# Optimization experiments

Measured on AMD Instinct MI355X. Metric: run time of the kernel, lower is better.

## Reference

```python
import jax, jax.numpy as jnp
import numpy as np

N = 100000
E = 3200000
F_IN = 128
H1, H2 = 32, 16
R = 8
G = 512  # number of graphs in batch


def setup_inputs() -> dict:
    key = jax.random.key(0)
    ks = jax.random.split(key, 12)
    x = jax.random.normal(ks[0], (N, F_IN), dtype=jnp.float32)
    edge_index = jax.random.randint(ks[1], (2, E), 0, N, dtype=jnp.int64)
    edge_attr = jax.random.randint(ks[2], (E,), 0, R, dtype=jnp.int64)
    batch = jnp.sort(jax.random.randint(ks[3], (N,), 0, G, dtype=jnp.int64))
    s1 = 1.0 / np.sqrt(F_IN)
    s2 = 1.0 / np.sqrt(H1)
    s3 = 1.0 / np.sqrt(H2)
    W1 = jax.random.uniform(ks[4], (R, F_IN, H1), jnp.float32, -s1, s1)
    root1 = jax.random.uniform(ks[5], (F_IN, H1), jnp.float32, -s1, s1)
    b1 = jnp.zeros((H1,), jnp.float32)
    W2 = jax.random.uniform(ks[6], (R, H1, H2), jnp.float32, -s2, s2)
    root2 = jax.random.uniform(ks[7], (H1, H2), jnp.float32, -s2, s2)
    b2 = jnp.zeros((H2,), jnp.float32)
    dense_w = jax.random.uniform(ks[8], (H2, 1), jnp.float32, -s3, s3)
    dense_b = jax.random.uniform(ks[9], (1,), jnp.float32, -s3, s3)
    return dict(x=x, edge_index=edge_index, edge_attr=edge_attr, batch=batch,
                W1=W1, root1=root1, b1=b1, W2=W2, root2=root2, b2=b2,
                dense_w=dense_w, dense_b=dense_b)


def rgcn_layer(x, W, root, b, src, dst, rel, num_rel):
    # Per-relation transform of all nodes: [N, R, out]
    xw = jnp.einsum('ni,rio->nro', x, W)
    msgs = xw[src, rel]                      # gather per edge: [E, out]
    seg = dst * num_rel + rel                # (node, relation) segment id
    nr = x.shape[0] * num_rel
    sums = jax.ops.segment_sum(msgs, seg, num_segments=nr)
    cnt = jax.ops.segment_sum(jnp.ones(src.shape, x.dtype), seg, num_segments=nr)
    mean = sums / jnp.maximum(cnt, 1.0)[:, None]
    agg = mean.reshape(x.shape[0], num_rel, -1).sum(axis=1)  # sum over relations
    return agg + x @ root + b


def reference(x, edge_index, edge_attr, batch, W1, root1, b1, W2, root2, b2, dense_w, dense_b):
    src, dst = edge_index[0], edge_index[1]
    rel = edge_attr
    h = jax.nn.relu(rgcn_layer(x, W1, root1, b1, src, dst, rel, R))
    # F.dropout is treated as identity (inference) for a deterministic reference
    h = jax.nn.relu(rgcn_layer(h, W2, root2, b2, src, dst, rel, R))
    pooled = jax.ops.segment_max(h, batch, num_segments=G)
    pooled = jnp.where(jnp.isfinite(pooled), pooled, 0.0)  # empty graphs -> 0
    return pooled @ dense_w + dense_b
```

## Files before the change

### kernel.cpp

```cpp
#include <hip/hip_runtime.h>
#include <hip/hip_bf16.h>

#define RNUM 8
#define HH1 32
#define HH2 16
#define FIN 128
#define BNODES 256
#define NBMAX 512
#define PCHUNK 8192
#define SORTCAP 11264

#define W1STR 136
#define W1ELTS (288 * W1STR)
#define W2STR 40
#define W2ELTS (144 * W2STR)

typedef short bf16x8 __attribute__((ext_vector_type(8)));
typedef float f32x4 __attribute__((ext_vector_type(4)));

__device__ inline bf16x8 cvt8r(float4 a, float4 b) {
  float tmp[8] = {a.x, a.y, a.z, a.w, b.x, b.y, b.z, b.w};
  bf16x8 r;
  #pragma unroll
  for (int j = 0; j < 8; ++j) {
    union { __hip_bfloat16 h; short s; } cv;
    cv.h = __float2bfloat16(tmp[j]);
    r[j] = cv.s;
  }
  return r;
}

__device__ inline bf16x8 cvt8relu(const float* __restrict__ p) {
  float tmp[8];
  *(float4*)tmp = *(const float4*)p;
  *(float4*)(tmp + 4) = *(const float4*)(p + 4);
  bf16x8 r;
  #pragma unroll
  for (int j = 0; j < 8; ++j) {
    union { __hip_bfloat16 h; short s; } cv;
    cv.h = __float2bfloat16(fmaxf(tmp[j], 0.f));
    r[j] = cv.s;
  }
  return r;
}

__device__ inline uint2 pack4bf(f32x4 v) {
  union { unsigned short u[4]; uint2 w; } pk;
  union { __hip_bfloat16 h; unsigned short s; } cv;
  cv.h = __float2bfloat16(v[0]); pk.u[0] = cv.s;
  cv.h = __float2bfloat16(v[1]); pk.u[1] = cv.s;
  cv.h = __float2bfloat16(v[2]); pk.u[2] = cv.s;
  cv.h = __float2bfloat16(v[3]); pk.u[3] = cv.s;
  return pk.w;
}

__global__ __launch_bounds__(256) void k_bhist(const int* __restrict__ ei,
    int* __restrict__ ghist, int E, int NB) {
  __shared__ int h[NBMAX];
  int t = threadIdx.x;
  for (int i = t; i < NBMAX; i += 256) h[i] = 0;
  __syncthreads();
  int base = blockIdx.x * 4096;
  #pragma unroll
  for (int j = 0; j < 16; ++j) {
    int e = base + j * 256 + t;
    if (e < E) atomicAdd(&h[ei[E + e] >> 8], 1);
  }
  __syncthreads();
  for (int i = t; i < NB; i += 256)
    if (h[i]) atomicAdd(&ghist[i], h[i]);
}

__global__ __launch_bounds__(NBMAX) void k_bscan(const int* __restrict__ ghist,
    int* __restrict__ bbase, int* __restrict__ gcursor, int NB, int E) {
  __shared__ int buf[NBMAX];
  int t = threadIdx.x;
  int v = (t < NB) ? ghist[t] : 0;
  buf[t] = v;
  __syncthreads();
  for (int d = 1; d < NBMAX; d <<= 1) {
    int w = (t >= d) ? buf[t - d] : 0;
    __syncthreads();
    buf[t] += w;
    __syncthreads();
  }
  if (t < NB) {
    int ex = buf[t] - v;
    bbase[t] = ex;
    gcursor[t] = ex;
  }
  if (t == 0) bbase[NB] = E;
}

__global__ __launch_bounds__(512) void k_part(const int* __restrict__ ei,
    const int* __restrict__ ea, int* __restrict__ gcursor,
    unsigned* __restrict__ ebuf, int E, int NB) {
  __shared__ unsigned reorder[PCHUNK];
  __shared__ unsigned short bkt[PCHUNK];
  __shared__ int hist[NBMAX], startl[NBMAX], cursor[NBMAX], gb[NBMAX], scanb[NBMAX];
  int t = threadIdx.x;
  int base = blockIdx.x * PCHUNK;
  int cn = min(PCHUNK, E - base);
  unsigned key[16];
  short bb[16];
  hist[t] = 0;
  __syncthreads();
  #pragma unroll
  for (int j = 0; j < 16; ++j) {
    int e = base + j * 512 + t;
    bb[j] = -1;
    if (e < E) {
      int src = ei[e], dst = ei[E + e], rel = ea[e];
      key[j] = ((unsigned)(dst & (BNODES - 1)) << 20) | ((unsigned)src << 3) | (unsigned)rel;
      int b = dst >> 8;
      bb[j] = (short)b;
      atomicAdd(&hist[b], 1);
    }
  }
  __syncthreads();
  int v = hist[t];
  scanb[t] = v;
  __syncthreads();
  for (int d = 1; d < NBMAX; d <<= 1) {
    int w = (t >= d) ? scanb[t - d] : 0;
    __syncthreads();
    scanb[t] += w;
    __syncthreads();
  }
  startl[t] = scanb[t] - v;
  cursor[t] = scanb[t] - v;
  __syncthreads();
  #pragma unroll
  for (int j = 0; j < 16; ++j) {
    if (bb[j] >= 0) {
      int pos = atomicAdd(&cursor[bb[j]], 1);
      reorder[pos] = key[j];
      bkt[pos] = (unsigned short)bb[j];
    }
  }
  __syncthreads();
  if (t < NB && hist[t] > 0) gb[t] = atomicAdd(&gcursor[t], hist[t]);
  __syncthreads();
  for (int p = t; p < cn; p += 512) {
    int b = bkt[p];
    ebuf[gb[b] + (p - startl[b])] = reorder[p];
  }
}

__global__ __launch_bounds__(512) void k_sort(const int* __restrict__ bbase,
    const unsigned* __restrict__ ebuf, unsigned* __restrict__ ebuf2,
    float* __restrict__ wbuf, int* __restrict__ rps, int* __restrict__ rpc,
    int NB) {
  __shared__ int hist[2048];
  __shared__ float invw[2048];
  __shared__ int dlc[256];
  __shared__ unsigned sorted[SORTCAP];
  int t = threadIdx.x;
  int b = blockIdx.x;
  int s = bbase[b], e = bbase[b + 1];
  int out_s = ((s + 7) & ~7) + (b << 11);
  for (int i = t; i < 2048; i += 512) hist[i] = 0;
  __syncthreads();
  for (int p = s + t; p < e; p += 512) {
    unsigned k = ebuf[p];
    atomicAdd(&hist[((k >> 20) << 3) | (k & 7u)], 1);
  }
  __syncthreads();
  for (int i = t; i < 2048; i += 512) {
    int c = hist[i];
    invw[i] = 1.0f / (float)(c > 1 ? c : 1);
  }
  __syncthreads();
  int pr[8];
  int cdl = 0, pc = 0;
  if (t < 256) {
    #pragma unroll
    for (int r = 0; r < 8; ++r) { pr[r] = cdl; cdl += hist[8 * t + r]; }
    pc = (cdl + 7) & ~7;
    dlc[t] = pc;
  }
  __syncthreads();
  for (int d = 1; d < 256; d <<= 1) {
    int w = (t < 256 && t >= d) ? dlc[t - d] : 0;
    __syncthreads();
    if (t < 256) dlc[t] += w;
    __syncthreads();
  }
  if (t < 256) {
    int ebase = dlc[t] - pc;
    #pragma unroll
    for (int r = 0; r < 8; ++r) hist[8 * t + r] = ebase + pr[r];
    rps[(b << 8) + t] = out_s + ebase;
    rpc[(b << 8) + t] = cdl;
  }
  __syncthreads();
  int ptot = dlc[255];
  if (ptot <= SORTCAP) {
    for (int p = t; p < ptot; p += 512) sorted[p] = 0xFFFFFFFFu;
    __syncthreads();
    for (int p = s + t; p < e; p += 512) {
      unsigned k = ebuf[p];
      int pos = atomicAdd(&hist[((k >> 20) << 3) | (k & 7u)], 1);
      sorted[pos] = k;
    }
    __syncthreads();
    for (int p = t; p < ptot; p += 512) {
      unsigned k = sorted[p];
      int o = out_s + p;
      if (k == 0xFFFFFFFFu) { ebuf2[o] = 0u; wbuf[o] = 0.f; }
      else { ebuf2[o] = k; wbuf[o] = invw[((k >> 20) << 3) | (k & 7u)]; }
    }
  } else {
    if (t < 256) {
      int ebase = dlc[t] - pc;
      for (int p = ebase + cdl; p < dlc[t]; ++p) {
        ebuf2[out_s + p] = 0u; wbuf[out_s + p] = 0.f;
      }
    }
    __syncthreads();
    for (int p = s + t; p < e; p += 512) {
      unsigned k = ebuf[p];
      int bin = ((k >> 20) << 3) | (k & 7u);
      int pos = atomicAdd(&hist[bin], 1);
      ebuf2[out_s + pos] = k;
      wbuf[out_s + pos] = invw[bin];
    }
  }
}

__global__ __launch_bounds__(256) void k_prepw(const float* __restrict__ W1,
    const float* __restrict__ root1, const float* __restrict__ W2,
    const float* __restrict__ root2, unsigned short* __restrict__ Wcat,
    unsigned short* __restrict__ W2cat) {
  int id = blockIdx.x * 256 + threadIdx.x;
  union { __hip_bfloat16 h; unsigned short u; } cv;
  if (id < W1ELTS) {
    int c = id / W1STR, kk = id - c * W1STR;
    float v = 0.f;
    if (kk < FIN)
      v = (c < 256) ? W1[((size_t)(c >> 5) * FIN + kk) * HH1 + (c & 31)]
                    : root1[(size_t)kk * HH1 + (c - 256)];
    cv.h = __float2bfloat16(v);
    Wcat[id] = cv.u;
  } else if (id < W1ELTS + W2ELTS) {
    int id2 = id - W1ELTS;
    int c = id2 / W2STR, kk = id2 - c * W2STR;
    float v = 0.f;
    if (kk < HH1)
      v = (c < 128) ? W2[((size_t)(c >> 4) * HH1 + kk) * HH2 + (c & 15)]
                    : root2[(size_t)kk * HH2 + (c - 128)];
    cv.h = __float2bfloat16(v);
    W2cat[id2] = cv.u;
  }
}

__global__ __launch_bounds__(384) void k_gemm1m(const float* __restrict__ x,
    const unsigned short* __restrict__ Wcat, const float* __restrict__ b1,
    __hip_bfloat16* __restrict__ xw, float* __restrict__ agg, int N, int nchunk) {
  int lane = threadIdx.x & 63;
  int wv = threadIdx.x >> 6;
  int g = lane >> 4, lc = lane & 15;
  int cj0 = wv * 3;
  bf16x8 Wf[3][4];
  #pragma unroll
  for (int j = 0; j < 3; ++j)
    #pragma unroll
    for (int ks = 0; ks < 4; ++ks)
      Wf[j][ks] = *(const bf16x8*)(Wcat + (size_t)((cj0 + j) * 16 + lc) * W1STR + ks * 32 + g * 8);

  for (int ch = blockIdx.x; ch < nchunk; ch += gridDim.x) {
    long base = (long)ch * 32;
    long r0 = base + lc;       if (r0 > N - 1) r0 = N - 1;
    long r1 = base + 16 + lc;  if (r1 > N - 1) r1 = N - 1;
    const float4* p0 = (const float4*)(x + r0 * FIN + g * 8);
    const float4* p1 = (const float4*)(x + r1 * FIN + g * 8);
    float4 raw[16];
    #pragma unroll
    for (int ks = 0; ks < 4; ++ks) {
      raw[2 * ks]     = p0[ks * 8];
      raw[2 * ks + 1] = p0[ks * 8 + 1];
    }
    #pragma unroll
    for (int ks = 0; ks < 4; ++ks) {
      raw[8 + 2 * ks]     = p1[ks * 8];
      raw[8 + 2 * ks + 1] = p1[ks * 8 + 1];
    }
    bf16x8 xf0[4], xf1[4];
    #pragma unroll
    for (int ks = 0; ks < 4; ++ks) {
      xf0[ks] = cvt8r(raw[2 * ks], raw[2 * ks + 1]);
      xf1[ks] = cvt8r(raw[8 + 2 * ks], raw[8 + 2 * ks + 1]);
    }
    f32x4 acc0[3], acc1[3];
    #pragma unroll
    for (int j = 0; j < 3; ++j) {
      acc0[j] = (f32x4){0.f, 0.f, 0.f, 0.f};
      acc1[j] = (f32x4){0.f, 0.f, 0.f, 0.f};
    }
    #pragma unroll
    for (int j = 0; j < 3; ++j)
      #pragma unroll
      for (int ks = 0; ks < 4; ++ks) {
        acc0[j] = __builtin_amdgcn_mfma_f32_16x16x32_bf16(Wf[j][ks], xf0[ks], acc0[j], 0, 0, 0);
        acc1[j] = __builtin_amdgcn_mfma_f32_16x16x32_bf16(Wf[j][ks], xf1[ks], acc1[j], 0, 0, 0);
      }
    long row0 = base + lc;
    if (row0 < N) {
      #pragma unroll
      for (int j = 0; j < 3; ++j) {
        int c0 = (cj0 + j) * 16 + 4 * g;
        if (c0 < 256) {
          *(uint2*)((unsigned short*)xw + row0 * 256 + c0) = pack4bf(acc0[j]);
        } else {
          float4 bb = *(const float4*)(b1 + (c0 - 256));
          float4 o = make_float4(acc0[j][0] + bb.x, acc0[j][1] + bb.y,
                                 acc0[j][2] + bb.z, acc0[j][3] + bb.w);
          *(float4*)(agg + row0 * HH1 + (c0 - 256)) = o;
        }
      }
    }
    long row1 = base + 16 + lc;
    if (row1 < N) {
      #pragma unroll
      for (int j = 0; j < 3; ++j) {
        int c0 = (cj0 + j) * 16 + 4 * g;
        if (c0 < 256) {
          *(uint2*)((unsigned short*)xw + row1 * 256 + c0) = pack4bf(acc1[j]);
        } else {
          float4 bb = *(const float4*)(b1 + (c0 - 256));
          float4 o = make_float4(acc1[j][0] + bb.x, acc1[j][1] + bb.y,
                                 acc1[j][2] + bb.z, acc1[j][3] + bb.w);
          *(float4*)(agg + row1 * HH1 + (c0 - 256)) = o;
        }
      }
    }
  }
}

__global__ __launch_bounds__(256) void k_agg1(const int* __restrict__ rps,
    const int* __restrict__ rpc, const unsigned* __restrict__ eb,
    const float* __restrict__ wb, const __hip_bfloat16* __restrict__ xw,
    float* __restrict__ agg, int N) {
  int d = blockIdx.x * 4 + (threadIdx.x >> 6);
  if (d >= N) return;
  int lane = threadIdx.x & 63;
  int h = lane & 31, half = lane >> 5;
  int s = rps[d];
  int cnt = rpc[d];
  float acc = 0.f;
  for (int j = half * 8; j < cnt; j += 16) {
    const unsigned* kp = eb + s + j;
    uint4 ka = *(const uint4*)kp;
    uint4 kb = *(const uint4*)(kp + 4);
    float4 wa = *(const float4*)(wb + s + j);
    float4 wc = *(const float4*)(wb + s + j + 4);
    unsigned ks[8] = {ka.x, ka.y, ka.z, ka.w, kb.x, kb.y, kb.z, kb.w};
    float ws[8] = {wa.x, wa.y, wa.z, wa.w, wc.x, wc.y, wc.z, wc.w};
    #pragma unroll
    for (int u = 0; u < 8; ++u) {
      unsigned idx = ks[u] & 0xFFFFFu;
      float v = __bfloat162float(xw[((size_t)idx << 5) + h]);
      acc = fmaf(ws[u], v, acc);
    }
  }
  acc += __shfl_xor(acc, 32);
  if (half == 0) agg[((size_t)d << 5) + h] += acc;
}

__global__ __launch_bounds__(384) void k_gemm2m(const float* __restrict__ agg1,
    const unsigned short* __restrict__ W2cat, const float* __restrict__ b2,
    __hip_bfloat16* __restrict__ xw, float* __restrict__ agg, int N) {
  __shared__ short WL[W2ELTS];
  __shared__ short XT[192 * 132];
  __shared__ float AG[192 * 20];
  int t = threadIdx.x;
  for (int i = t; i < W2ELTS / 8; i += 384)
    ((uint4*)WL)[i] = ((const uint4*)W2cat)[i];
  __syncthreads();
  int lane = t & 63;
  int wv = t >> 6;
  int g = lane >> 4, lc = lane & 15;
  long nb = (long)blockIdx.x * 192 + wv * 32;
  f32x4 acc[2][9];
  #pragma unroll
  for (int m = 0; m < 2; ++m)
    #pragma unroll
    for (int j = 0; j < 9; ++j)
      acc[m][j] = (f32x4){0.f, 0.f, 0.f, 0.f};
  long rowA0 = nb + lc;       if (rowA0 > N - 1) rowA0 = N - 1;
  long rowA1 = nb + 16 + lc;  if (rowA1 > N - 1) rowA1 = N - 1;
  bf16x8 a0 = cvt8relu(agg1 + rowA0 * HH1 + g * 8);
  bf16x8 a1 = cvt8relu(agg1 + rowA1 * HH1 + g * 8);
  #pragma unroll
  for (int j = 0; j < 9; ++j) {
    bf16x8 bf = *(const bf16x8*)(WL + (16 * j + lc) * W2STR + g * 8);
    acc[0][j] = __builtin_amdgcn_mfma_f32_16x16x32_bf16(bf, a0, acc[0][j], 0, 0, 0);
    acc[1][j] = __builtin_amdgcn_mfma_f32_16x16x32_bf16(bf, a1, acc[1][j], 0, 0, 0);
  }
  #pragma unroll
  for (int m = 0; m < 2; ++m) {
    int lrow = wv * 32 + 16 * m + lc;
    #pragma unroll
    for (int j = 0; j < 8; ++j)
      *(uint2*)(XT + lrow * 132 + 16 * j + 4 * g) = pack4bf(acc[m][j]);
    float4 bb = *(const float4*)(b2 + 4 * g);
    *(float4*)(AG + lrow * 20 + 4 * g) =
        make_float4(acc[m][8][0] + bb.x, acc[m][8][1] + bb.y,
                    acc[m][8][2] + bb.z, acc[m][8][3] + bb.w);
  }
  __syncthreads();
  long base = (long)blockIdx.x * 192;
  for (int i = t; i < 6144; i += 384) {
    int row = i >> 5, u = i & 31;
    long grow = base + row;
    if (grow < N)
      *(uint2*)((unsigned short*)xw + grow * 128 + u * 4) = *(const uint2*)(XT + row * 132 + u * 4);
  }
  for (int i = t; i < 768; i += 384) {
    int row = i >> 2, q = i & 3;
    long grow = base + row;
    if (grow < N)
      *(float4*)(agg + grow * HH2 + q * 4) = *(const float4*)(AG + row * 20 + q * 4);
  }
}

__global__ __launch_bounds__(256) void k_agg2f(const int* __restrict__ rps,
    const int* __restrict__ rpc, const unsigned* __restrict__ eb,
    const float* __restrict__ wb, const __hip_bfloat16* __restrict__ xw,
    const float* __restrict__ agg2r, const int* __restrict__ batch,
    unsigned* __restrict__ pooled, int N) {
  int d = blockIdx.x * 4 + (threadIdx.x >> 6);
  if (d >= N) return;
  int lane = threadIdx.x & 63;
  int h = lane & 15, q = lane >> 4;
  int s = rps[d];
  int cnt = rpc[d];
  float acc = 0.f;
  for (int j = q * 8; j < cnt; j += 32) {
    const unsigned* kp = eb + s + j;
    uint4 ka = *(const uint4*)kp;
    uint4 kb = *(const uint4*)(kp + 4);
    float4 wa = *(const float4*)(wb + s + j);
    float4 wc = *(const float4*)(wb + s + j + 4);
    unsigned ks[8] = {ka.x, ka.y, ka.z, ka.w, kb.x, kb.y, kb.z, kb.w};
    float ws[8] = {wa.x, wa.y, wa.z, wa.w, wc.x, wc.y, wc.z, wc.w};
    #pragma unroll
    for (int u = 0; u < 8; ++u) {
      unsigned idx = ks[u] & 0xFFFFFu;
      float v = __bfloat162float(xw[((size_t)idx << 4) + h]);
      acc = fmaf(ws[u], v, acc);
    }
  }
  acc += __shfl_xor(acc, 32);
  acc += __shfl_xor(acc, 16);
  if (q == 0) {
    float v = fmaxf(acc + agg2r[((size_t)d << 4) + h], 0.f);
    atomicMax(&pooled[batch[d] * HH2 + h], __float_as_uint(v));
  }
}

__global__ __launch_bounds__(256) void k_dense(const float* __restrict__ pooled,
    const float* __restrict__ dw, const float* __restrict__ db,
    float* __restrict__ out, int Gn) {
  int g = blockIdx.x * 256 + threadIdx.x;
  if (g < Gn) {
    float s = db[0];
    #pragma unroll
    for (int h = 0; h < HH2; ++h) s += pooled[(size_t)g * HH2 + h] * dw[h];
    out[g] = s;
  }
}

extern "C" void kernel_launch(void* const* d_in, const int* in_sizes, int n_in,
                              void* d_out, int out_size, void* d_ws, size_t ws_size,
                              hipStream_t stream) {
  const float* x     = (const float*)d_in[0];
  const int*   ei    = (const int*)d_in[1];
  const int*   ea    = (const int*)d_in[2];
  const int*   batch = (const int*)d_in[3];
  const float* W1    = (const float*)d_in[4];
  const float* root1 = (const float*)d_in[5];
  const float* b1    = (const float*)d_in[6];
  const float* W2    = (const float*)d_in[7];
  const float* root2 = (const float*)d_in[8];
  const float* b2    = (const float*)d_in[9];
  const float* dw    = (const float*)d_in[10];
  const float* db    = (const float*)d_in[11];
  float* out = (float*)d_out;

  const int N  = in_sizes[0] / FIN;
  const int E  = in_sizes[2];
  const int Gn = out_size;
  const int NB = (N + BNODES - 1) / BNODES;

  char* ws = (char*)d_ws;
  size_t off = 0;
  auto walloc = [&](size_t bytes) -> void* {
    void* p = (void*)(ws + off);
    off += (bytes + 255) & ~(size_t)255;
    return p;
  };
  const size_t EP = (size_t)E + (size_t)NBMAX * 2048 + 64;
  int*            ghist   = (int*)            walloc((size_t)NBMAX * 4);
  int*            bbase   = (int*)            walloc(((size_t)NBMAX + 1) * 4);
  int*            gcursor = (int*)            walloc((size_t)NBMAX * 4);
  unsigned*       ebuf    = (unsigned*)       walloc((size_t)E * 4);
  unsigned*       ebuf2   = (unsigned*)       walloc(EP * 4);
  float*          wbuf    = (float*)          walloc(EP * 4);
  int*            rps     = (int*)            walloc((size_t)NBMAX * 256 * 4);
  int*            rpc     = (int*)            walloc((size_t)NBMAX * 256 * 4);
  unsigned short* Wcat    = (unsigned short*) walloc((size_t)W1ELTS * 2);
  unsigned short* W2cat   = (unsigned short*) walloc((size_t)W2ELTS * 2);
  __hip_bfloat16* xw1     = (__hip_bfloat16*) walloc((size_t)N * RNUM * HH1 * 2);
  float*          agg1    = (float*)          walloc((size_t)N * HH1 * 4);
  __hip_bfloat16* xw2     = (__hip_bfloat16*) walloc((size_t)N * RNUM * HH2 * 2);
  float*          agg2r   = (float*)          walloc((size_t)N * HH2 * 4);
  unsigned*       pooled  = (unsigned*)       walloc((size_t)Gn * HH2 * 4);

  hipMemsetAsync(ghist, 0, (size_t)NBMAX * 4, stream);
  hipMemsetAsync(pooled, 0, (size_t)Gn * HH2 * 4, stream);

  k_prepw<<<(W1ELTS + W2ELTS + 255) / 256, 256, 0, stream>>>(W1, root1, W2, root2, Wcat, W2cat);
  k_bhist<<<(E + 4095) / 4096, 256, 0, stream>>>(ei, ghist, E, NB);
  k_bscan<<<1, NBMAX, 0, stream>>>(ghist, bbase, gcursor, NB, E);
  k_part<<<(E + PCHUNK - 1) / PCHUNK, 512, 0, stream>>>(ei, ea, gcursor, ebuf, E, NB);
  k_sort<<<NB, 512, 0, stream>>>(bbase, ebuf, ebuf2, wbuf, rps, rpc, NB);

  {
    int nchunk = (N + 31) / 32;
    k_gemm1m<<<nchunk, 384, 0, stream>>>(x, Wcat, b1, xw1, agg1, N, nchunk);
  }
  k_agg1<<<(N + 3) / 4, 256, 0, stream>>>(rps, rpc, ebuf2, wbuf, xw1, agg1, N);
  k_gemm2m<<<(N + 191) / 192, 384, 0, stream>>>(agg1, W2cat, b2, xw2, agg2r, N);
  k_agg2f<<<(N + 3) / 4, 256, 0, stream>>>(rps, rpc, ebuf2, wbuf, xw2,
                                           agg2r, batch, pooled, N);
  k_dense<<<(Gn + 255) / 256, 256, 0, stream>>>((const float*)pooled, dw, db, out, Gn);
}
```

Before: 276.3 us.

## Fuse bucket sort and layer-1 GEMM into one launch with block specialization

Merges the per-bucket edge sort kernel and the first-layer MFMA GEMM into a single launch. The first NB blocks do the sort and the remaining 512 blocks run a grid-strided GEMM, so the two independent stages can overlap and one launch is saved. The sort also drops its shared-memory staging path and always scatters directly to global memory, which frees LDS for occupancy but gives less coalesced writes. Fixing the GEMM grid at 512 blocks with 384 active threads out of 512 may leave some compute idle.

```diff
diff --git a/kernel.cpp b/kernel.cpp
--- a/kernel.cpp
+++ b/kernel.cpp
@@ -8,7 +8,7 @@
 #define BNODES 256
 #define NBMAX 512
 #define PCHUNK 8192
-#define SORTCAP 11264
+#define GEMMB 512
 
 #define W1STR 136
 #define W1ELTS (288 * W1STR)
@@ -147,74 +147,58 @@
   }
 }
 
-__global__ __launch_bounds__(512) void k_sort(const int* __restrict__ bbase,
-    const unsigned* __restrict__ ebuf, unsigned* __restrict__ ebuf2,
-    float* __restrict__ wbuf, int* __restrict__ rps, int* __restrict__ rpc,
-    int NB) {
+__global__ __launch_bounds__(512) void k_fuse2(
+    const int* __restrict__ bbase, const unsigned* __restrict__ ebuf,
+    unsigned* __restrict__ ebuf2, float* __restrict__ wbuf,
+    int* __restrict__ rps, int* __restrict__ rpc, int NB,
+    const float* __restrict__ x, const unsigned short* __restrict__ Wcat,
+    const float* __restrict__ b1, __hip_bfloat16* __restrict__ xw,
+    float* __restrict__ agg, int N, int nchunk) {
   __shared__ int hist[2048];
   __shared__ float invw[2048];
   __shared__ int dlc[256];
-  __shared__ unsigned sorted[SORTCAP];
   int t = threadIdx.x;
-  int b = blockIdx.x;
-  int s = bbase[b], e = bbase[b + 1];
-  int out_s = ((s + 7) & ~7) + (b << 11);
-  for (int i = t; i < 2048; i += 512) hist[i] = 0;
-  __syncthreads();
-  for (int p = s + t; p < e; p += 512) {
-    unsigned k = ebuf[p];
-    atomicAdd(&hist[((k >> 20) << 3) | (k & 7u)], 1);
-  }
-  __syncthreads();
-  for (int i = t; i < 2048; i += 512) {
-    int c = hist[i];
-    invw[i] = 1.0f / (float)(c > 1 ? c : 1);
-  }
-  __syncthreads();
-  int pr[8];
-  int cdl = 0, pc = 0;
-  if (t < 256) {
-    #pragma unroll
-    for (int r = 0; r < 8; ++r) { pr[r] = cdl; cdl += hist[8 * t + r]; }
-    pc = (cdl + 7) & ~7;
-    dlc[t] = pc;
-  }
-  __syncthreads();
-  for (int d = 1; d < 256; d <<= 1) {
-    int w = (t < 256 && t >= d) ? dlc[t - d] : 0;
-    __syncthreads();
-    if (t < 256) dlc[t] += w;
-    __syncthreads();
-  }
-  if (t < 256) {
-    int ebase = dlc[t] - pc;
-    #pragma unroll
-    for (int r = 0; r < 8; ++r) hist[8 * t + r] = ebase + pr[r];
-    rps[(b << 8) + t] = out_s + ebase;
-    rpc[(b << 8) + t] = cdl;
-  }
-  __syncthreads();
-  int ptot = dlc[255];
-  if (ptot <= SORTCAP) {
-    for (int p = t; p < ptot; p += 512) sorted[p] = 0xFFFFFFFFu;
+
+  if (blockIdx.x < NB) {
+    int b = blockIdx.x;
+    int s = bbase[b], e = bbase[b + 1];
+    int out_s = ((s + 7) & ~7) + (b << 11);
+    for (int i = t; i < 2048; i += 512) hist[i] = 0;
     __syncthreads();
     for (int p = s + t; p < e; p += 512) {
       unsigned k = ebuf[p];
-      int pos = atomicAdd(&hist[((k >> 20) << 3) | (k & 7u)], 1);
-      sorted[pos] = k;
-    }
-    __syncthreads();
-    for (int p = t; p < ptot; p += 512) {
-      unsigned k = sorted[p];
-      int o = out_s + p;
-      if (k == 0xFFFFFFFFu) { ebuf2[o] = 0u; wbuf[o] = 0.f; }
-      else { ebuf2[o] = k; wbuf[o] = invw[((k >> 20) << 3) | (k & 7u)]; }
-    }
-  } else {
+      atomicAdd(&hist[((k >> 20) << 3) | (k & 7u)], 1);
+    }
+    __syncthreads();
+    for (int i = t; i < 2048; i += 512) {
+      int c = hist[i];
+      invw[i] = 1.0f / (float)(c > 1 ? c : 1);
+    }
+    __syncthreads();
+    int pr[8];
+    int cdl = 0, pc = 0;
+    if (t < 256) {
+      #pragma unroll
+      for (int r = 0; r < 8; ++r) { pr[r] = cdl; cdl += hist[8 * t + r]; }
+      pc = (cdl + 7) & ~7;
+      dlc[t] = pc;
+    }
+    __syncthreads();
+    for (int d = 1; d < 256; d <<= 1) {
+      int w = (t < 256 && t >= d) ? dlc[t - d] : 0;
+      __syncthreads();
+      if (t < 256) dlc[t] += w;
+      __syncthreads();
+    }
     if (t < 256) {
       int ebase = dlc[t] - pc;
+      #pragma unroll
+      for (int r = 0; r < 8; ++r) hist[8 * t + r] = ebase + pr[r];
+      rps[(b << 8) + t] = out_s + ebase;
+      rpc[(b << 8) + t] = cdl;
       for (int p = ebase + cdl; p < dlc[t]; ++p) {
-        ebuf2[out_s + p] = 0u; wbuf[out_s + p] = 0.f;
+        ebuf2[out_s + p] = 0u;
+        wbuf[out_s + p] = 0.f;
       }
     }
     __syncthreads();
@@ -224,6 +208,88 @@
       int pos = atomicAdd(&hist[bin], 1);
       ebuf2[out_s + pos] = k;
       wbuf[out_s + pos] = invw[bin];
+    }
+    return;
+  }
+
+  if (t >= 384) return;
+  int lane = t & 63;
+  int wv = t >> 6;
+  int g = lane >> 4, lc = lane & 15;
+  int cj0 = wv * 3;
+  bf16x8 Wf[3][4];
+  #pragma unroll
+  for (int j = 0; j < 3; ++j)
+    #pragma unroll
+    for (int ks = 0; ks < 4; ++ks)
+      Wf[j][ks] = *(const bf16x8*)(Wcat + (size_t)((cj0 + j) * 16 + lc) * W1STR + ks * 32 + g * 8);
+
+  int gstride = gridDim.x - NB;
+  for (int ch = blockIdx.x - NB; ch < nchunk; ch += gstride) {
+    long base = (long)ch * 32;
+    long r0 = base + lc;       if (r0 > N - 1) r0 = N - 1;
+    long r1 = base + 16 + lc;  if (r1 > N - 1) r1 = N - 1;
+    const float4* p0 = (const float4*)(x + r0 * FIN + g * 8);
+    const float4* p1 = (const float4*)(x + r1 * FIN + g * 8);
+    float4 raw[16];
+    #pragma unroll
+    for (int ks = 0; ks < 4; ++ks) {
+      raw[2 * ks]     = p0[ks * 8];
+      raw[2 * ks + 1] = p0[ks * 8 + 1];
+    }
+    #pragma unroll
+    for (int ks = 0; ks < 4; ++ks) {
+      raw[8 + 2 * ks]     = p1[ks * 8];
+      raw[8 + 2 * ks + 1] = p1[ks * 8 + 1];
+    }
+    bf16x8 xf0[4], xf1[4];
+    #pragma unroll
+    for (int ks = 0; ks < 4; ++ks) {
+      xf0[ks] = cvt8r(raw[2 * ks], raw[2 * ks + 1]);
+      xf1[ks] = cvt8r(raw[8 + 2 * ks], raw[8 + 2 * ks + 1]);
+    }
+    f32x4 acc0[3], acc1[3];
+    #pragma unroll
+    for (int j = 0; j < 3; ++j) {
+      acc0[j] = (f32x4){0.f, 0.f, 0.f, 0.f};
+      acc1[j] = (f32x4){0.f, 0.f, 0.f, 0.f};
+    }
+    #pragma unroll
+    for (int j = 0; j < 3; ++j)
+      #pragma unroll
+      for (int ks = 0; ks < 4; ++ks) {
+        acc0[j] = __builtin_amdgcn_mfma_f32_16x16x32_bf16(Wf[j][ks], xf0[ks], acc0[j], 0, 0, 0);
+        acc1[j] = __builtin_amdgcn_mfma_f32_16x16x32_bf16(Wf[j][ks], xf1[ks], acc1[j], 0, 0, 0);
+      }
+    long row0 = base + lc;
+    if (row0 < N) {
+      #pragma unroll
+      for (int j = 0; j < 3; ++j) {
+        int c0 = (cj0 + j) * 16 + 4 * g;
+        if (c0 < 256) {
+          *(uint2*)((unsigned short*)xw + row0 * 256 + c0) = pack4bf(acc0[j]);
+        } else {
+          float4 bb = *(const float4*)(b1 + (c0 - 256));
+          float4 o = make_float4(acc0[j][0] + bb.x, acc0[j][1] + bb.y,
+                                 acc0[j][2] + bb.z, acc0[j][3] + bb.w);
+          *(float4*)(agg + row0 * HH1 + (c0 - 256)) = o;
+        }
+      }
+    }
+    long row1 = base + 16 + lc;
+    if (row1 < N) {
+      #pragma unroll
+      for (int j = 0; j < 3; ++j) {
+        int c0 = (cj0 + j) * 16 + 4 * g;
+        if (c0 < 256) {
+          *(uint2*)((unsigned short*)xw + row1 * 256 + c0) = pack4bf(acc1[j]);
+        } else {
+          float4 bb = *(const float4*)(b1 + (c0 - 256));
+          float4 o = make_float4(acc1[j][0] + bb.x, acc1[j][1] + bb.y,
+                                 acc1[j][2] + bb.z, acc1[j][3] + bb.w);
+          *(float4*)(agg + row1 * HH1 + (c0 - 256)) = o;
+        }
+      }
     }
   }
 }
@@ -254,89 +320,6 @@
   }
 }
 
-__global__ __launch_bounds__(384) void k_gemm1m(const float* __restrict__ x,
-    const unsigned short* __restrict__ Wcat, const float* __restrict__ b1,
-    __hip_bfloat16* __restrict__ xw, float* __restrict__ agg, int N, int nchunk) {
-  int lane = threadIdx.x & 63;
-  int wv = threadIdx.x >> 6;
-  int g = lane >> 4, lc = lane & 15;
-  int cj0 = wv * 3;
-  bf16x8 Wf[3][4];
-  #pragma unroll
-  for (int j = 0; j < 3; ++j)
-    #pragma unroll
-    for (int ks = 0; ks < 4; ++ks)
-      Wf[j][ks] = *(const bf16x8*)(Wcat + (size_t)((cj0 + j) * 16 + lc) * W1STR + ks * 32 + g * 8);
-
-  for (int ch = blockIdx.x; ch < nchunk; ch += gridDim.x) {
-    long base = (long)ch * 32;
-    long r0 = base + lc;       if (r0 > N - 1) r0 = N - 1;
-    long r1 = base + 16 + lc;  if (r1 > N - 1) r1 = N - 1;
-    const float4* p0 = (const float4*)(x + r0 * FIN + g * 8);
-    const float4* p1 = (const float4*)(x + r1 * FIN + g * 8);
-    float4 raw[16];
-    #pragma unroll
-    for (int ks = 0; ks < 4; ++ks) {
-      raw[2 * ks]     = p0[ks * 8];
-      raw[2 * ks + 1] = p0[ks * 8 + 1];
-    }
-    #pragma unroll
-    for (int ks = 0; ks < 4; ++ks) {
-      raw[8 + 2 * ks]     = p1[ks * 8];
-      raw[8 + 2 * ks + 1] = p1[ks * 8 + 1];
-    }
-    bf16x8 xf0[4], xf1[4];
-    #pragma unroll
-    for (int ks = 0; ks < 4; ++ks) {
-      xf0[ks] = cvt8r(raw[2 * ks], raw[2 * ks + 1]);
-      xf1[ks] = cvt8r(raw[8 + 2 * ks], raw[8 + 2 * ks + 1]);
-    }
-    f32x4 acc0[3], acc1[3];
-    #pragma unroll
-    for (int j = 0; j < 3; ++j) {
-      acc0[j] = (f32x4){0.f, 0.f, 0.f, 0.f};
-      acc1[j] = (f32x4){0.f, 0.f, 0.f, 0.f};
-    }
-    #pragma unroll
-    for (int j = 0; j < 3; ++j)
-      #pragma unroll
-      for (int ks = 0; ks < 4; ++ks) {
-        acc0[j] = __builtin_amdgcn_mfma_f32_16x16x32_bf16(Wf[j][ks], xf0[ks], acc0[j], 0, 0, 0);
-        acc1[j] = __builtin_amdgcn_mfma_f32_16x16x32_bf16(Wf[j][ks], xf1[ks], acc1[j], 0, 0, 0);
-      }
-    long row0 = base + lc;
-    if (row0 < N) {
-      #pragma unroll
-      for (int j = 0; j < 3; ++j) {
-        int c0 = (cj0 + j) * 16 + 4 * g;
-        if (c0 < 256) {
-          *(uint2*)((unsigned short*)xw + row0 * 256 + c0) = pack4bf(acc0[j]);
-        } else {
-          float4 bb = *(const float4*)(b1 + (c0 - 256));
-          float4 o = make_float4(acc0[j][0] + bb.x, acc0[j][1] + bb.y,
-                                 acc0[j][2] + bb.z, acc0[j][3] + bb.w);
-          *(float4*)(agg + row0 * HH1 + (c0 - 256)) = o;
-        }
-      }
-    }
-    long row1 = base + 16 + lc;
-    if (row1 < N) {
-      #pragma unroll
-      for (int j = 0; j < 3; ++j) {
-        int c0 = (cj0 + j) * 16 + 4 * g;
-        if (c0 < 256) {
-          *(uint2*)((unsigned short*)xw + row1 * 256 + c0) = pack4bf(acc1[j]);
-        } else {
-          float4 bb = *(const float4*)(b1 + (c0 - 256));
-          float4 o = make_float4(acc1[j][0] + bb.x, acc1[j][1] + bb.y,
-                                 acc1[j][2] + bb.z, acc1[j][3] + bb.w);
-          *(float4*)(agg + row1 * HH1 + (c0 - 256)) = o;
-        }
-      }
-    }
-  }
-}
-
 __global__ __launch_bounds__(256) void k_agg1(const int* __restrict__ rps,
     const int* __restrict__ rpc, const unsigned* __restrict__ eb,
     const float* __restrict__ wb, const __hip_bfloat16* __restrict__ xw,
@@ -524,11 +507,11 @@
   k_bhist<<<(E + 4095) / 4096, 256, 0, stream>>>(ei, ghist, E, NB);
   k_bscan<<<1, NBMAX, 0, stream>>>(ghist, bbase, gcursor, NB, E);
   k_part<<<(E + PCHUNK - 1) / PCHUNK, 512, 0, stream>>>(ei, ea, gcursor, ebuf, E, NB);
-  k_sort<<<NB, 512, 0, stream>>>(bbase, ebuf, ebuf2, wbuf, rps, rpc, NB);
 
   {
     int nchunk = (N + 31) / 32;
-    k_gemm1m<<<nchunk, 384, 0, stream>>>(x, Wcat, b1, xw1, agg1, N, nchunk);
+    k_fuse2<<<NB + GEMMB, 512, 0, stream>>>(bbase, ebuf, ebuf2, wbuf, rps, rpc, NB,
+                                            x, Wcat, b1, xw1, agg1, N, nchunk);
   }
   k_agg1<<<(N + 3) / 4, 256, 0, stream>>>(rps, rpc, ebuf2, wbuf, xw1, agg1, N);
   k_gemm2m<<<(N + 191) / 192, 384, 0, stream>>>(agg1, W2cat, b2, xw2, agg2r, N);
```

Result: slower. 309.7 us (+12.1%).
